# Optimization experiments

Hardware: AMD Instinct MI355X
Metric: run time of the kernel (lower is better)

## Reference

```python
import jax, jax.numpy as jnp
import numpy as np
from jax import lax

B, C, H, W = 8, 64, 64, 64
C8 = C // 8
EPS = 1e-5


def setup_inputs() -> dict:
    key = jax.random.key(0)
    ks = jax.random.split(key, 10)
    s = lambda *sh: 0.02
    inp = {
        "x": jax.random.normal(ks[0], (B, C, H, W), dtype=jnp.float32),
        "conv_b_w": jax.random.normal(ks[1], (C8, C), dtype=jnp.float32) * 0.05,
        "conv_b_b": jnp.zeros((C8,), jnp.float32),
        "conv_c_w": jax.random.normal(ks[2], (C8, C), dtype=jnp.float32) * 0.05,
        "conv_c_b": jnp.zeros((C8,), jnp.float32),
        "conv_d_w": jax.random.normal(ks[3], (C, C), dtype=jnp.float32) * 0.05,
        "conv_d_b": jnp.zeros((C,), jnp.float32),
        "alpha": jnp.zeros((1,), jnp.float32) + 0.1,  # learned PAM scale
        "beta": jnp.zeros((1,), jnp.float32) + 0.1,   # learned CAM scale
        "conv_w": jax.random.normal(ks[4], (2 * C, C, 3, 3), dtype=jnp.float32) * 0.02,
        "conv_bias": jnp.zeros((2 * C,), jnp.float32),
        "bn_gamma": jnp.ones((2 * C,), jnp.float32),
        "bn_beta": jnp.zeros((2 * C,), jnp.float32),
    }
    return inp


def _conv1x1(x, w, b):
    # x: [B,C,H,W], w: [O,C] -> [B,O,H,W]
    return jnp.einsum('oc,bchw->bohw', w, x) + b[None, :, None, None]


def _forward(x, conv_b_w, conv_b_b, conv_c_w, conv_c_b, conv_d_w, conv_d_b,
             alpha, beta, conv_w, conv_bias, bn_gamma, bn_beta):
    b, c, h, w = x.shape
    n = h * w
    # ---- Position Attention Module ----
    feat_b = _conv1x1(x, conv_b_w, conv_b_b).reshape(b, C8, n)   # [B,C8,N]
    feat_c = _conv1x1(x, conv_c_w, conv_c_b).reshape(b, C8, n)   # [B,C8,N]
    # torch: bmm(feat_b^T [B,N,C8], feat_c [B,C8,N]) -> [B,N,N]
    attn_s = jax.nn.softmax(jnp.einsum('bcn,bcm->bnm', feat_b, feat_c), axis=-1)
    feat_d = _conv1x1(x, conv_d_w, conv_d_b).reshape(b, c, n)    # [B,C,N]
    # torch: bmm(feat_d, attn_s^T) -> out[b,c,n] = sum_m feat_d[b,c,m]*attn[b,n,m]
    feat_e = jnp.einsum('bcm,bnm->bcn', feat_d, attn_s).reshape(b, c, h, w)
    x = alpha[0] * feat_e + x
    # ---- Channel Attention Module ----
    fa = x.reshape(b, c, n)                                      # [B,C,N]
    att = jnp.einsum('bcn,bdn->bcd', fa, fa)                     # [B,C,C]
    att_new = jnp.max(att, axis=-1, keepdims=True) - att
    att = jax.nn.softmax(att_new, axis=-1)
    fe = jnp.einsum('bcd,bdn->bcn', att, fa).reshape(b, c, h, w)
    x = beta[0] * fe + x
    # ---- conv3x3 + BN (batch stats) + ReLU + maxpool(2,2,pad=(1,0)) ----
    out = lax.conv_general_dilated(x, conv_w, (1, 1), ((1, 1), (1, 1)),
                                   dimension_numbers=('NCHW', 'OIHW', 'NCHW'))
    out = out + conv_bias[None, :, None, None]
    mean = jnp.mean(out, axis=(0, 2, 3), keepdims=True)
    var = jnp.var(out, axis=(0, 2, 3), keepdims=True)
    out = (out - mean) * lax.rsqrt(var + EPS)
    out = out * bn_gamma[None, :, None, None] + bn_beta[None, :, None, None]
    out = jax.nn.relu(out)
    # MaxPool2d(kernel=2, stride=2, padding=(1,0)): -inf padding on height only
    out = lax.reduce_window(out, -jnp.inf, lax.max,
                            (1, 1, 2, 2), (1, 1, 2, 2),
                            ((0, 0), (0, 0), (1, 1), (0, 0)))
    return out


def reference(x, conv_b_w, conv_b_b, conv_c_w, conv_c_b, conv_d_w, conv_d_b,
              alpha, beta, conv_w, conv_bias, bn_gamma, bn_beta):
    return _forward(x, conv_b_w, conv_b_b, conv_c_w, conv_c_b, conv_d_w, conv_d_b,
                    alpha, beta, conv_w, conv_bias, bn_gamma, bn_beta)
```

## Files before the change

kernel.cpp:

```cpp
#include <hip/hip_runtime.h>

using f32x4  = __attribute__((ext_vector_type(4))) float;
using bf16x8 = __attribute__((ext_vector_type(8))) short;
using u32x4  = __attribute__((ext_vector_type(4))) unsigned int;
using u32x2  = __attribute__((ext_vector_type(2))) unsigned int;
typedef unsigned short u16;

__device__ __forceinline__ u16 f2bf(float f) {
  unsigned u = __float_as_uint(f);
  unsigned r = (u + 0x7FFFu + ((u >> 16) & 1u)) >> 16;
  return (u16)r;
}

__global__ void __launch_bounds__(256) k1_conv1x1(
    const float* __restrict__ x, const float* __restrict__ wB, const float* __restrict__ bB,
    const float* __restrict__ wC, const float* __restrict__ bC,
    const float* __restrict__ wD, const float* __restrict__ bD,
    u16* __restrict__ featBb, u16* __restrict__ featCb, u16* __restrict__ featD,
    const float* __restrict__ cw, u16* __restrict__ wb) {
  const int t = threadIdx.x;
  const int b = blockIdx.y;
  const int z = blockIdx.z;
  if (z == 3) {
    int gid = (b * 16 + blockIdx.x) * 256 + t;
#pragma unroll
    for (int k = 0; k < 3; ++k) {
      int F = gid + k * 32768;
      if (F < 73728) {
        int j = F & 7, lane = (F >> 3) & 63, T = F >> 9;
        int tap = T >> 4, g = (T >> 1) & 7, kc = T & 1;
        int l16 = lane & 15, quad = lane >> 4;
        int oc = g * 16 + l16, ic = kc * 32 + quad * 8 + j;
        wb[F] = f2bf(cw[(oc * 64 + ic) * 9 + tap]);
      }
    }
    return;
  }
  __shared__ float W[2048];
  __shared__ float Bias[32];
  const int n = blockIdx.x * 256 + t;
  if (z == 0) {
    for (int i = t; i < 512; i += 256) W[i] = wB[i];
    for (int i = t; i < 512; i += 256) W[512 + i] = wC[i];
    if (t < 8) Bias[t] = bB[t];
    if (t >= 8 && t < 16) Bias[t] = bC[t - 8];
  } else {
    const float* wsrc = wD + (z - 1) * 2048;
    for (int i = t; i < 2048; i += 256) W[i] = wsrc[i];
    if (t < 32) Bias[t] = bD[(z - 1) * 32 + t];
  }
  __syncthreads();
  float xv[64];
#pragma unroll
  for (int c = 0; c < 64; ++c) xv[c] = x[((b * 64 + c) << 12) + n];
  if (z == 0) {
    float o[16];
#pragma unroll
    for (int k = 0; k < 16; ++k) {
      f32x4 s = {0.f, 0.f, 0.f, 0.f};
#pragma unroll
      for (int cq = 0; cq < 16; ++cq) {
        f32x4 wv = *(const f32x4*)&W[k * 64 + cq * 4];
        f32x4 xq = {xv[cq * 4], xv[cq * 4 + 1], xv[cq * 4 + 2], xv[cq * 4 + 3]};
        s += wv * xq;
      }
      o[k] = Bias[k] + s[0] + s[1] + s[2] + s[3];
    }
    int base = ((b << 12) + n) * 8;
    u32x4 pb, pc;
#pragma unroll
    for (int i = 0; i < 4; ++i) {
      pb[i] = (unsigned)f2bf(o[2 * i]) | ((unsigned)f2bf(o[2 * i + 1]) << 16);
      pc[i] = (unsigned)f2bf(o[8 + 2 * i]) | ((unsigned)f2bf(o[8 + 2 * i + 1]) << 16);
    }
    *(u32x4*)&featBb[base] = pb;
    *(u32x4*)&featCb[base] = pc;
  } else {
#pragma unroll 4
    for (int k = 0; k < 32; ++k) {
      f32x4 s = {0.f, 0.f, 0.f, 0.f};
#pragma unroll
      for (int cq = 0; cq < 16; ++cq) {
        f32x4 wv = *(const f32x4*)&W[k * 64 + cq * 4];
        f32x4 xq = {xv[cq * 4], xv[cq * 4 + 1], xv[cq * 4 + 2], xv[cq * 4 + 3]};
        s += wv * xq;
      }
      float val = Bias[k] + s[0] + s[1] + s[2] + s[3];
      featD[((b * 64 + (z - 1) * 32 + k) << 12) + n] = f2bf(val);
    }
  }
}

__global__ void __launch_bounds__(256) k2_pam_part(
    const u16* __restrict__ fBb, const u16* __restrict__ fCb, const u16* __restrict__ fD,
    u16* __restrict__ numPart, float* __restrict__ denPart) {
  __shared__ u16 Kf[128 * 8];
  __shared__ u16 Df[64 * 132];
  __shared__ u16 Ps4[4][2][16 * 72];
  const int t = threadIdx.x, b = blockIdx.y, z = blockIdx.z;
  const int w = t >> 6, lane = t & 63, quad = lane >> 4, l16 = lane & 15;
  const int nb = blockIdx.x * 256 + w * 64;
  u16* myPs = &Ps4[w][0][0];

  bf16x8 bq[4];
#pragma unroll
  for (int j = 0; j < 4; ++j) {
    bq[j] = *(const bf16x8*)&fBb[(((b << 12) + nb + j * 16 + l16) << 3)];
    if (quad != 0) bq[j] = (bf16x8)(short)0;
  }

  f32x4 acc[4][4];
#pragma unroll
  for (int ct = 0; ct < 4; ++ct)
#pragma unroll
    for (int j = 0; j < 4; ++j) acc[ct][j] = (f32x4){0.f, 0.f, 0.f, 0.f};
  float denp[4] = {0.f, 0.f, 0.f, 0.f};
  const int mz = z << 10;

  for (int ch = 0; ch < 8; ++ch) {
    const int m0 = mz + (ch << 7);
    __syncthreads();
    if (t < 128) *(u32x4*)&Kf[t * 8] = *(const u32x4*)&fCb[(((b << 12) + m0 + t) << 3)];
#pragma unroll
    for (int h = 0; h < 4; ++h) {
      int idx = h * 256 + t;
      int r = idx >> 4, mo = (idx & 15) << 3;
      *(u32x4*)&Df[r * 132 + mo] = *(const u32x4*)&fD[((b * 64 + r) << 12) + m0 + mo];
    }
    __syncthreads();
#pragma unroll
    for (int sub = 0; sub < 2; ++sub) {
      const int ms = sub * 64;
#pragma unroll
      for (int jp = 0; jp < 2; ++jp) {
#pragma unroll
        for (int mt = 0; mt < 4; ++mt) {
          bf16x8 af = *(const bf16x8*)&Kf[(ms + mt * 16 + l16) * 8];
#pragma unroll
          for (int jj = 0; jj < 2; ++jj) {
            const int j = jp * 2 + jj;
            f32x4 zero = {0.f, 0.f, 0.f, 0.f};
            f32x4 s = __builtin_amdgcn_mfma_f32_16x16x32_bf16(af, bq[j], zero, 0, 0, 0);
            float e0 = __expf(s[0]), e1 = __expf(s[1]), e2 = __expf(s[2]), e3 = __expf(s[3]);
            denp[j] += (e0 + e1) + (e2 + e3);
            u32x2 pk;
            pk[0] = __builtin_amdgcn_perm(__float_as_uint(e1), __float_as_uint(e0), 0x07060302u);
            pk[1] = __builtin_amdgcn_perm(__float_as_uint(e3), __float_as_uint(e2), 0x07060302u);
            *(u32x2*)&myPs[jj * 1152 + l16 * 72 + mt * 16 + quad * 4] = pk;
          }
        }
#pragma unroll
        for (int kc = 0; kc < 2; ++kc) {
          bf16x8 bv0 = *(const bf16x8*)&myPs[0 * 1152 + l16 * 72 + kc * 32 + quad * 8];
          bf16x8 bv1 = *(const bf16x8*)&myPs[1 * 1152 + l16 * 72 + kc * 32 + quad * 8];
#pragma unroll
          for (int ct = 0; ct < 4; ++ct) {
            bf16x8 av = *(const bf16x8*)&Df[(ct * 16 + l16) * 132 + ms + kc * 32 + quad * 8];
            acc[ct][jp * 2]     = __builtin_amdgcn_mfma_f32_16x16x32_bf16(av, bv0, acc[ct][jp * 2], 0, 0, 0);
            acc[ct][jp * 2 + 1] = __builtin_amdgcn_mfma_f32_16x16x32_bf16(av, bv1, acc[ct][jp * 2 + 1], 0, 0, 0);
          }
        }
      }
    }
  }
#pragma unroll
  for (int j = 0; j < 4; ++j) {
    denp[j] += __shfl_xor(denp[j], 16);
    denp[j] += __shfl_xor(denp[j], 32);
  }
  const int zb = z * 8 + b;
#pragma unroll
  for (int ct = 0; ct < 4; ++ct)
#pragma unroll
    for (int j = 0; j < 4; ++j)
#pragma unroll
      for (int r = 0; r < 4; ++r) {
        int c = ct * 16 + quad * 4 + r;
        numPart[((zb * 64 + c) << 12) + nb + j * 16 + l16] = (u16)(__float_as_uint(acc[ct][j][r]) >> 16);
      }
  if (quad == 0)
#pragma unroll
    for (int j = 0; j < 4; ++j) denPart[(zb << 12) + nb + j * 16 + l16] = denp[j];
}

__global__ void __launch_bounds__(256) k3_gram(
    const u16* __restrict__ numPart, const float* __restrict__ denPart,
    const float* __restrict__ x, const float* __restrict__ alpha,
    float* __restrict__ x1, float* __restrict__ attPart) {
  __shared__ float X[64 * 132];
  __shared__ float Dinv[128];
  const int t = threadIdx.x, b = blockIdx.y, cx = blockIdx.x;
  const int n0 = cx * 128;
  if (t < 128) {
    float den = 0.f;
#pragma unroll
    for (int z = 0; z < 4; ++z) den += denPart[(((z * 8 + b) << 12)) + n0 + t];
    Dinv[t] = alpha[0] / den;
  }
  __syncthreads();
  for (int idx = t; idx < 4096; idx += 256) {
    int row = idx >> 6, cp = (idx & 63) * 2;
    int gi = ((b * 64 + row) << 12) + n0 + cp;
    float num0 = 0.f, num1 = 0.f;
#pragma unroll
    for (int z = 0; z < 4; ++z) {
      unsigned v = *(const unsigned*)&numPart[(((z * 8 + b) * 64 + row) << 12) + n0 + cp];
      num0 += __uint_as_float(v << 16);
      num1 += __uint_as_float(v & 0xFFFF0000u);
    }
    float v0 = num0 * Dinv[cp] + x[gi];
    float v1 = num1 * Dinv[cp + 1] + x[gi + 1];
    X[row * 132 + cp] = v0;
    X[row * 132 + cp + 1] = v1;
    x1[gi] = v0;
    x1[gi + 1] = v1;
  }
  __syncthreads();
  const int cg = t >> 4, dg = t & 15;
  f32x4 acc[4][4];
#pragma unroll
  for (int i = 0; i < 4; ++i)
#pragma unroll
    for (int k = 0; k < 4; ++k) acc[i][k] = (f32x4){0.f, 0.f, 0.f, 0.f};
  for (int nq0 = 0; nq0 < 32; ++nq0) {
    int nq = (nq0 + dg) & 31;
    f32x4 a[4], bb[4];
#pragma unroll
    for (int i = 0; i < 4; ++i) a[i] = *(const f32x4*)&X[(cg * 4 + i) * 132 + nq * 4];
#pragma unroll
    for (int k = 0; k < 4; ++k) bb[k] = *(const f32x4*)&X[(dg * 4 + k) * 132 + nq * 4];
#pragma unroll
    for (int i = 0; i < 4; ++i)
#pragma unroll
      for (int k = 0; k < 4; ++k) acc[i][k] += a[i] * bb[k];
  }
#pragma unroll
  for (int i = 0; i < 4; ++i)
#pragma unroll
    for (int k = 0; k < 4; ++k) {
      f32x4 s = acc[i][k];
      attPart[((b * 32 + cx) * 64 + cg * 4 + i) * 64 + dg * 4 + k] = s[0] + s[1] + s[2] + s[3];
    }
}

__global__ void __launch_bounds__(256) k4_softmax(const float* __restrict__ attPart, float* __restrict__ attP) {
  const int b = blockIdx.y, t = threadIdx.x;
  const int c = (blockIdx.x << 2) + (t >> 6), d = t & 63;
  float v = 0.f;
  for (int p = 0; p < 32; ++p) v += attPart[((b * 32 + p) * 64 + c) * 64 + d];
  float mn = v;
#pragma unroll
  for (int off = 1; off < 64; off <<= 1) mn = fminf(mn, __shfl_xor(mn, off));
  float e = __expf(mn - v);
  float sum = e;
#pragma unroll
  for (int off = 1; off < 64; off <<= 1) sum += __shfl_xor(sum, off);
  attP[(b * 64 + c) * 64 + d] = e / sum;
}

__global__ void __launch_bounds__(256, 1) k5_apply(
    const float* __restrict__ attP, const float* __restrict__ x1,
    const float* __restrict__ beta, u16* __restrict__ x2b) {
  __shared__ float A[64 * 68];
  const int t = threadIdx.x, b = blockIdx.y;
  for (int idx = t; idx < 4096; idx += 256) A[(idx >> 6) * 68 + (idx & 63)] = attP[(b << 12) + idx];
  __syncthreads();
  const int n = blockIdx.x * 256 + t;
  float xv[64];
#pragma unroll
  for (int d = 0; d < 64; ++d) xv[d] = x1[((b * 64 + d) << 12) + n];
  const float bv = beta[0];
  u16* orow = x2b + (((size_t)(b << 12) + n) << 6);
#pragma unroll 2
  for (int cg = 0; cg < 8; ++cg) {
    unsigned pk[4];
#pragma unroll
    for (int ci = 0; ci < 8; ++ci) {
      int c = cg * 8 + ci;
      f32x4 s = {0.f, 0.f, 0.f, 0.f};
#pragma unroll
      for (int dq = 0; dq < 16; ++dq) {
        f32x4 avv = *(const f32x4*)&A[c * 68 + dq * 4];
        f32x4 xq = {xv[dq * 4], xv[dq * 4 + 1], xv[dq * 4 + 2], xv[dq * 4 + 3]};
        s += avv * xq;
      }
      float fe = s[0] + s[1] + s[2] + s[3];
      float val = bv * fe + xv[c];
      unsigned h = f2bf(val);
      if ((ci & 1) == 0) pk[ci >> 1] = h;
      else pk[ci >> 1] |= h << 16;
    }
    *(u32x4*)&orow[cg * 8] = (u32x4){pk[0], pk[1], pk[2], pk[3]};
  }
}

__global__ void __launch_bounds__(256) k6_mfma(const u16* __restrict__ x2b, const u16* __restrict__ wb,
                                               float* __restrict__ y) {
  __shared__ u16 Xl[3 * 66 * 72];
  const int t = threadIdx.x, b = blockIdx.y, h = blockIdx.x;
  for (int idx = t; idx < 3 * 66 * 8; idx += 256) {
    int r = idx / 528;
    int rem = idx - r * 528;
    int c = rem >> 3, icq = rem & 7;
    int gy = h - 1 + r, gx = c - 1;
    u32x4 v = {0u, 0u, 0u, 0u};
    if (gy >= 0 && gy < 64 && gx >= 0 && gx < 64)
      v = *(const u32x4*)&x2b[(((size_t)(b << 6 | gy) << 6) + gx) * 64 + icq * 8];
    *(u32x4*)&Xl[(r * 66 + c) * 72 + icq * 8] = v;
  }
  __syncthreads();
  const int w = t >> 6, lane = t & 63, quad = lane >> 4, l16 = lane & 15;
  const int mBase = (w & 1) * 64;
  const int og = (w & 1) * 4;
  const int nBase = (w >> 1) * 32;
  f32x4 acc[4][2];
#pragma unroll
  for (int ot = 0; ot < 4; ++ot)
#pragma unroll
    for (int nt = 0; nt < 2; ++nt) acc[ot][nt] = (f32x4){0.f, 0.f, 0.f, 0.f};
#pragma unroll 3
  for (int tap = 0; tap < 9; ++tap) {
    const int dy = tap / 3, dx = tap - dy * 3;
    bf16x8 af[4][2];
#pragma unroll
    for (int ot = 0; ot < 4; ++ot)
#pragma unroll
      for (int kc = 0; kc < 2; ++kc)
        af[ot][kc] = *(const bf16x8*)&wb[((((tap * 8 + og + ot) * 2 + kc) << 6) + lane) << 3];
#pragma unroll
    for (int nt = 0; nt < 2; ++nt) {
      const int prow = dy * 66 + nBase + nt * 16 + l16 + dx;
#pragma unroll
      for (int kc = 0; kc < 2; ++kc) {
        bf16x8 bv = *(const bf16x8*)&Xl[prow * 72 + kc * 32 + quad * 8];
#pragma unroll
        for (int ot = 0; ot < 4; ++ot)
          acc[ot][nt] = __builtin_amdgcn_mfma_f32_16x16x32_bf16(af[ot][kc], bv, acc[ot][nt], 0, 0, 0);
      }
    }
  }
#pragma unroll
  for (int ot = 0; ot < 4; ++ot)
#pragma unroll
    for (int nt = 0; nt < 2; ++nt)
#pragma unroll
      for (int r = 0; r < 4; ++r) {
        int oc = mBase + ot * 16 + quad * 4 + r;
        int pix = nBase + nt * 16 + l16;
        y[((b * 128 + oc) << 12) + (h << 6) + pix] = acc[ot][nt][r];
      }
}

__global__ void __launch_bounds__(256) k7_part(const float* __restrict__ y, float* __restrict__ pstats) {
  const int ch = blockIdx.x, q = blockIdx.y, t = threadIdx.x;
  float s = 0.f, ss = 0.f;
#pragma unroll
  for (int bb = 0; bb < 2; ++bb) {
    const float* p = y + (((q * 2 + bb) * 128 + ch) << 12);
#pragma unroll
    for (int i = 0; i < 16; ++i) { float v = p[i * 256 + t]; s += v; ss += v * v; }
  }
#pragma unroll
  for (int off = 1; off < 64; off <<= 1) { s += __shfl_xor(s, off); ss += __shfl_xor(ss, off); }
  __shared__ float rs[4], rss[4];
  if ((t & 63) == 0) { rs[t >> 6] = s; rss[t >> 6] = ss; }
  __syncthreads();
  if (t == 0) {
    pstats[ch * 8 + q * 2]     = rs[0] + rs[1] + rs[2] + rs[3];
    pstats[ch * 8 + q * 2 + 1] = rss[0] + rss[1] + rss[2] + rss[3];
  }
}

__global__ void __launch_bounds__(256) k8_pool(const float* __restrict__ y, const float* __restrict__ pstats,
                                               const float* __restrict__ gamma, const float* __restrict__ bbeta,
                                               float* __restrict__ out) {
  const int bc = blockIdx.x;
  const int ch = bc & 127;
  float S = 0.f, SS = 0.f;
#pragma unroll
  for (int q = 0; q < 4; ++q) { S += pstats[ch * 8 + q * 2]; SS += pstats[ch * 8 + q * 2 + 1]; }
  const float mean = S * (1.f / 32768.f);
  const float var = SS * (1.f / 32768.f) - mean * mean;
  const float sc = gamma[ch] * rsqrtf(var + 1e-5f);
  const float sh = bbeta[ch] - mean * sc;
  const float* p = y + (bc << 12);
  float* op = out + bc * (33 * 32);
  for (int i = threadIdx.x; i < 33 * 32; i += 256) {
    int oh = i >> 5, ow = i & 31;
    int r0 = 2 * oh - 1, r1 = 2 * oh;
    float m = 0.f;
    if (r0 >= 0) {
      m = fmaxf(m, p[r0 * 64 + 2 * ow] * sc + sh);
      m = fmaxf(m, p[r0 * 64 + 2 * ow + 1] * sc + sh);
    }
    if (r1 <= 63) {
      m = fmaxf(m, p[r1 * 64 + 2 * ow] * sc + sh);
      m = fmaxf(m, p[r1 * 64 + 2 * ow + 1] * sc + sh);
    }
    op[i] = m;
  }
}

extern "C" void kernel_launch(void* const* d_in, const int* in_sizes, int n_in,
                              void* d_out, int out_size, void* d_ws, size_t ws_size,
                              hipStream_t stream) {
  const float* x      = (const float*)d_in[0];
  const float* wB     = (const float*)d_in[1];
  const float* bB     = (const float*)d_in[2];
  const float* wC     = (const float*)d_in[3];
  const float* bC     = (const float*)d_in[4];
  const float* wD     = (const float*)d_in[5];
  const float* bD     = (const float*)d_in[6];
  const float* alpha  = (const float*)d_in[7];
  const float* beta   = (const float*)d_in[8];
  const float* cw     = (const float*)d_in[9];
  const float* gamma  = (const float*)d_in[11];
  const float* bnbeta = (const float*)d_in[12];

  char* ws = (char*)d_ws;
  u16*   featBb  = (u16*)  (ws + 0);
  u16*   featCb  = (u16*)  (ws + 524288);
  u16*   fDb     = (u16*)  (ws + 1048576);
  u16*   x2b     = (u16*)  (ws + 0);
  float* x1      = (float*)(ws + 5242880);
  u16*   numPart = (u16*)  (ws + 13631488);
  float* y       = (float*)(ws + 13631488);
  float* denPart = (float*)(ws + 30408704);
  float* attPart = (float*)(ws + 30932992);
  float* attP    = (float*)(ws + 35127296);
  u16*   wb      = (u16*)  (ws + 35258368);
  float* pstats  = (float*)(ws + 35405824);
  float* outp    = (float*)d_out;

  k1_conv1x1<<<dim3(16, 8, 4), 256, 0, stream>>>(x, wB, bB, wC, bC, wD, bD, featBb, featCb, fDb, cw, wb);
  k2_pam_part<<<dim3(16, 8, 4), 256, 0, stream>>>(featBb, featCb, fDb, numPart, denPart);
  k3_gram<<<dim3(32, 8), 256, 0, stream>>>(numPart, denPart, x, alpha, x1, attPart);
  k4_softmax<<<dim3(16, 8), 256, 0, stream>>>(attPart, attP);
  k5_apply<<<dim3(16, 8), 256, 0, stream>>>(attP, x1, beta, x2b);
  k6_mfma<<<dim3(64, 8), 256, 0, stream>>>(x2b, wb, y);
  k7_part<<<dim3(128, 4), 256, 0, stream>>>(y, pstats);
  k8_pool<<<dim3(1024), 256, 0, stream>>>(y, pstats, gamma, bnbeta, outp);
}
```

Before: 216.1 us.

## Merge conv1x1 z-slices into one block and halve PAM query tile per wave

k1 now has each block compute featB, featC and all 64 featD channels from a single load of x, instead of spreading them over three z-slices that each reload x; the weight-repack slice moves to z==1. k2 shrinks each wave's query tile from 64 to 32 columns and doubles the grid to 32x8x4 blocks, aiming for more parallelism and lower register pressure, but it reloads the K and D chunks twice as often overall. Launch bounds of (256,1) are added to k1 and k3, which may raise register use at the cost of occupancy.

```diff
diff --git a/kernel.cpp b/kernel.cpp
--- a/kernel.cpp
+++ b/kernel.cpp
@@ -12,7 +12,7 @@
   return (u16)r;
 }
 
-__global__ void __launch_bounds__(256) k1_conv1x1(
+__global__ void __launch_bounds__(256, 1) k1_conv1x1(
     const float* __restrict__ x, const float* __restrict__ wB, const float* __restrict__ bB,
     const float* __restrict__ wC, const float* __restrict__ bC,
     const float* __restrict__ wD, const float* __restrict__ bD,
@@ -20,8 +20,7 @@
     const float* __restrict__ cw, u16* __restrict__ wb) {
   const int t = threadIdx.x;
   const int b = blockIdx.y;
-  const int z = blockIdx.z;
-  if (z == 3) {
+  if (blockIdx.z == 1) {
     int gid = (b * 16 + blockIdx.x) * 256 + t;
 #pragma unroll
     for (int k = 0; k < 3; ++k) {
@@ -36,24 +35,20 @@
     }
     return;
   }
-  __shared__ float W[2048];
-  __shared__ float Bias[32];
+  __shared__ float W[80 * 64];
+  __shared__ float Bias[80];
+  for (int i = t; i < 512; i += 256) W[i] = wB[i];
+  for (int i = t; i < 512; i += 256) W[512 + i] = wC[i];
+  for (int i = t; i < 4096; i += 256) W[1024 + i] = wD[i];
+  if (t < 8) Bias[t] = bB[t];
+  else if (t < 16) Bias[t] = bC[t - 8];
+  else if (t < 80) Bias[t] = bD[t - 16];
+  __syncthreads();
   const int n = blockIdx.x * 256 + t;
-  if (z == 0) {
-    for (int i = t; i < 512; i += 256) W[i] = wB[i];
-    for (int i = t; i < 512; i += 256) W[512 + i] = wC[i];
-    if (t < 8) Bias[t] = bB[t];
-    if (t >= 8 && t < 16) Bias[t] = bC[t - 8];
-  } else {
-    const float* wsrc = wD + (z - 1) * 2048;
-    for (int i = t; i < 2048; i += 256) W[i] = wsrc[i];
-    if (t < 32) Bias[t] = bD[(z - 1) * 32 + t];
-  }
-  __syncthreads();
   float xv[64];
 #pragma unroll
   for (int c = 0; c < 64; ++c) xv[c] = x[((b * 64 + c) << 12) + n];
-  if (z == 0) {
+  {
     float o[16];
 #pragma unroll
     for (int k = 0; k < 16; ++k) {
@@ -75,19 +70,18 @@
     }
     *(u32x4*)&featBb[base] = pb;
     *(u32x4*)&featCb[base] = pc;
-  } else {
+  }
 #pragma unroll 4
-    for (int k = 0; k < 32; ++k) {
-      f32x4 s = {0.f, 0.f, 0.f, 0.f};
-#pragma unroll
-      for (int cq = 0; cq < 16; ++cq) {
-        f32x4 wv = *(const f32x4*)&W[k * 64 + cq * 4];
-        f32x4 xq = {xv[cq * 4], xv[cq * 4 + 1], xv[cq * 4 + 2], xv[cq * 4 + 3]};
-        s += wv * xq;
-      }
-      float val = Bias[k] + s[0] + s[1] + s[2] + s[3];
-      featD[((b * 64 + (z - 1) * 32 + k) << 12) + n] = f2bf(val);
-    }
+  for (int k = 0; k < 64; ++k) {
+    f32x4 s = {0.f, 0.f, 0.f, 0.f};
+#pragma unroll
+    for (int cq = 0; cq < 16; ++cq) {
+      f32x4 wv = *(const f32x4*)&W[(16 + k) * 64 + cq * 4];
+      f32x4 xq = {xv[cq * 4], xv[cq * 4 + 1], xv[cq * 4 + 2], xv[cq * 4 + 3]};
+      s += wv * xq;
+    }
+    float val = Bias[16 + k] + s[0] + s[1] + s[2] + s[3];
+    featD[((b * 64 + k) << 12) + n] = f2bf(val);
   }
 }
 
@@ -99,22 +93,22 @@
   __shared__ u16 Ps4[4][2][16 * 72];
   const int t = threadIdx.x, b = blockIdx.y, z = blockIdx.z;
   const int w = t >> 6, lane = t & 63, quad = lane >> 4, l16 = lane & 15;
-  const int nb = blockIdx.x * 256 + w * 64;
+  const int nb = blockIdx.x * 128 + w * 32;
   u16* myPs = &Ps4[w][0][0];
 
-  bf16x8 bq[4];
-#pragma unroll
-  for (int j = 0; j < 4; ++j) {
+  bf16x8 bq[2];
+#pragma unroll
+  for (int j = 0; j < 2; ++j) {
     bq[j] = *(const bf16x8*)&fBb[(((b << 12) + nb + j * 16 + l16) << 3)];
     if (quad != 0) bq[j] = (bf16x8)(short)0;
   }
 
-  f32x4 acc[4][4];
+  f32x4 acc[4][2];
 #pragma unroll
   for (int ct = 0; ct < 4; ++ct)
 #pragma unroll
-    for (int j = 0; j < 4; ++j) acc[ct][j] = (f32x4){0.f, 0.f, 0.f, 0.f};
-  float denp[4] = {0.f, 0.f, 0.f, 0.f};
+    for (int j = 0; j < 2; ++j) acc[ct][j] = (f32x4){0.f, 0.f, 0.f, 0.f};
+  float denp[2] = {0.f, 0.f};
   const int mz = z << 10;
 
   for (int ch = 0; ch < 8; ++ch) {
@@ -132,39 +126,35 @@
     for (int sub = 0; sub < 2; ++sub) {
       const int ms = sub * 64;
 #pragma unroll
-      for (int jp = 0; jp < 2; ++jp) {
-#pragma unroll
-        for (int mt = 0; mt < 4; ++mt) {
-          bf16x8 af = *(const bf16x8*)&Kf[(ms + mt * 16 + l16) * 8];
-#pragma unroll
-          for (int jj = 0; jj < 2; ++jj) {
-            const int j = jp * 2 + jj;
-            f32x4 zero = {0.f, 0.f, 0.f, 0.f};
-            f32x4 s = __builtin_amdgcn_mfma_f32_16x16x32_bf16(af, bq[j], zero, 0, 0, 0);
-            float e0 = __expf(s[0]), e1 = __expf(s[1]), e2 = __expf(s[2]), e3 = __expf(s[3]);
-            denp[j] += (e0 + e1) + (e2 + e3);
-            u32x2 pk;
-            pk[0] = __builtin_amdgcn_perm(__float_as_uint(e1), __float_as_uint(e0), 0x07060302u);
-            pk[1] = __builtin_amdgcn_perm(__float_as_uint(e3), __float_as_uint(e2), 0x07060302u);
-            *(u32x2*)&myPs[jj * 1152 + l16 * 72 + mt * 16 + quad * 4] = pk;
-          }
+      for (int mt = 0; mt < 4; ++mt) {
+        bf16x8 af = *(const bf16x8*)&Kf[(ms + mt * 16 + l16) * 8];
+#pragma unroll
+        for (int j = 0; j < 2; ++j) {
+          f32x4 zero = {0.f, 0.f, 0.f, 0.f};
+          f32x4 s = __builtin_amdgcn_mfma_f32_16x16x32_bf16(af, bq[j], zero, 0, 0, 0);
+          float e0 = __expf(s[0]), e1 = __expf(s[1]), e2 = __expf(s[2]), e3 = __expf(s[3]);
+          denp[j] += (e0 + e1) + (e2 + e3);
+          u32x2 pk;
+          pk[0] = __builtin_amdgcn_perm(__float_as_uint(e1), __float_as_uint(e0), 0x07060302u);
+          pk[1] = __builtin_amdgcn_perm(__float_as_uint(e3), __float_as_uint(e2), 0x07060302u);
+          *(u32x2*)&myPs[j * 1152 + l16 * 72 + mt * 16 + quad * 4] = pk;
         }
-#pragma unroll
-        for (int kc = 0; kc < 2; ++kc) {
-          bf16x8 bv0 = *(const bf16x8*)&myPs[0 * 1152 + l16 * 72 + kc * 32 + quad * 8];
-          bf16x8 bv1 = *(const bf16x8*)&myPs[1 * 1152 + l16 * 72 + kc * 32 + quad * 8];
-#pragma unroll
-          for (int ct = 0; ct < 4; ++ct) {
-            bf16x8 av = *(const bf16x8*)&Df[(ct * 16 + l16) * 132 + ms + kc * 32 + quad * 8];
-            acc[ct][jp * 2]     = __builtin_amdgcn_mfma_f32_16x16x32_bf16(av, bv0, acc[ct][jp * 2], 0, 0, 0);
-            acc[ct][jp * 2 + 1] = __builtin_amdgcn_mfma_f32_16x16x32_bf16(av, bv1, acc[ct][jp * 2 + 1], 0, 0, 0);
-          }
+      }
+#pragma unroll
+      for (int kc = 0; kc < 2; ++kc) {
+        bf16x8 bv0 = *(const bf16x8*)&myPs[0 * 1152 + l16 * 72 + kc * 32 + quad * 8];
+        bf16x8 bv1 = *(const bf16x8*)&myPs[1 * 1152 + l16 * 72 + kc * 32 + quad * 8];
+#pragma unroll
+        for (int ct = 0; ct < 4; ++ct) {
+          bf16x8 av = *(const bf16x8*)&Df[(ct * 16 + l16) * 132 + ms + kc * 32 + quad * 8];
+          acc[ct][0] = __builtin_amdgcn_mfma_f32_16x16x32_bf16(av, bv0, acc[ct][0], 0, 0, 0);
+          acc[ct][1] = __builtin_amdgcn_mfma_f32_16x16x32_bf16(av, bv1, acc[ct][1], 0, 0, 0);
         }
       }
     }
   }
 #pragma unroll
-  for (int j = 0; j < 4; ++j) {
+  for (int j = 0; j < 2; ++j) {
     denp[j] += __shfl_xor(denp[j], 16);
     denp[j] += __shfl_xor(denp[j], 32);
   }
@@ -172,7 +162,7 @@
 #pragma unroll
   for (int ct = 0; ct < 4; ++ct)
 #pragma unroll
-    for (int j = 0; j < 4; ++j)
+    for (int j = 0; j < 2; ++j)
 #pragma unroll
       for (int r = 0; r < 4; ++r) {
         int c = ct * 16 + quad * 4 + r;
@@ -180,10 +170,10 @@
       }
   if (quad == 0)
 #pragma unroll
-    for (int j = 0; j < 4; ++j) denPart[(zb << 12) + nb + j * 16 + l16] = denp[j];
-}
-
-__global__ void __launch_bounds__(256) k3_gram(
+    for (int j = 0; j < 2; ++j) denPart[(zb << 12) + nb + j * 16 + l16] = denp[j];
+}
+
+__global__ void __launch_bounds__(256, 1) k3_gram(
     const u16* __restrict__ numPart, const float* __restrict__ denPart,
     const float* __restrict__ x, const float* __restrict__ alpha,
     float* __restrict__ x1, float* __restrict__ attPart) {
@@ -432,8 +422,8 @@
   float* pstats  = (float*)(ws + 35405824);
   float* outp    = (float*)d_out;
 
-  k1_conv1x1<<<dim3(16, 8, 4), 256, 0, stream>>>(x, wB, bB, wC, bC, wD, bD, featBb, featCb, fDb, cw, wb);
-  k2_pam_part<<<dim3(16, 8, 4), 256, 0, stream>>>(featBb, featCb, fDb, numPart, denPart);
+  k1_conv1x1<<<dim3(16, 8, 2), 256, 0, stream>>>(x, wB, bB, wC, bC, wD, bD, featBb, featCb, fDb, cw, wb);
+  k2_pam_part<<<dim3(32, 8, 4), 256, 0, stream>>>(featBb, featCb, fDb, numPart, denPart);
   k3_gram<<<dim3(32, 8), 256, 0, stream>>>(numPart, denPart, x, alpha, x1, attPart);
   k4_softmax<<<dim3(16, 8), 256, 0, stream>>>(attPart, attP);
   k5_apply<<<dim3(16, 8), 256, 0, stream>>>(attP, x1, beta, x2b);
```

Measured after the change: 230.0 us. +6.4%, slower.
